# Kernel optimization log

Measured on AMD Instinct MI355X. Metric: run time of the kernel, lower is better.

## Reference

```python
import jax, jax.numpy as jnp
import numpy as np

NDIM = 3
IMG_SIZE = (192, 192, 192)
CPS = (5, 5, 5)
CP_GRID = (42, 42, 42)


def bspline_kernel_1d(stride):
    # cubic B-spline sampled at (i - radius)/stride, length 4*stride-1
    n = 4 * stride - 1
    t = np.abs((np.arange(n) - n // 2) / float(stride))
    vals = np.where(t < 1.0, 2.0 / 3.0 + (0.5 * t - 1.0) * t ** 2,
                    np.where(t < 2.0, -((t - 2.0) ** 3) / 6.0, 0.0))
    return jnp.asarray(vals, dtype=jnp.float32)


def conv_transpose1d_lastaxis(x, kernel, stride, padding):
    # depthwise transposed conv along last axis; same kernel for every channel,
    # so fold all leading dims into the batch and use a single-channel conv
    # with lhs_dilation (equivalent to conv_transpose; kernel is symmetric).
    shp = x.shape
    K = kernel.shape[0]
    x2 = x.reshape(-1, 1, shp[-1])  # [N, C=1, L]
    w = kernel.reshape(1, 1, K)     # [O, I, W]
    pad = K - 1 - padding
    y = jax.lax.conv_general_dilated(
        x2, w, window_strides=(1,), padding=[(pad, pad)],
        lhs_dilation=(stride,), dimension_numbers=("NCW", "OIW", "NCW"))
    return y.reshape(shp[:-1] + (y.shape[-1],))


def setup_inputs() -> dict:
    key = jax.random.key(0)
    v = jax.random.normal(key, (4, NDIM) + CP_GRID, dtype=jnp.float32)
    return {"v": v}


def reference(v) -> jnp.ndarray:
    kernels = [bspline_kernel_1d(s) for s in CPS]
    for i in range(NDIM):
        k = kernels[i]
        s = CPS[i]
        p = (k.shape[0] - 1) // 2
        x = jnp.moveaxis(v, i + 2, -1)
        x = conv_transpose1d_lastaxis(x, k, s, p)
        v = jnp.moveaxis(x, -1, i + 2)
    # crop: slice(s, s + img_size) per spatial dim
    slicer = (slice(None), slice(None)) + tuple(
        slice(CPS[i], CPS[i] + IMG_SIZE[i]) for i in range(NDIM))
    return v[slicer]
```

## Files before the change

kernel.cpp:

```cpp
#include <hip/hip_runtime.h>
#include <hip/hip_bf16.h>


#define CPN 42
#define IMG 192
#define TXX 6
#define TYY 6
#define NCX 5
#define NCY 5
#define NCZ 42
#define SXS 44
#define NTHREADS 256
#define ZBS 80
#define POOLF (TXX * TYY * ZBS)

struct WTabC { double w[5][4]; };
constexpr WTabC make_wb() {
  WTabC t{};
  for (int r = 0; r < 5; ++r) {
    double f = (double)r / 5.0;
    double g = (double)(5 - r) / 5.0;
    t.w[r][0] = g * g * g / 6.0;
    t.w[r][1] = 2.0 / 3.0 + (0.5 * f - 1.0) * f * f;
    t.w[r][2] = 2.0 / 3.0 + (0.5 * g - 1.0) * g * g;
    t.w[r][3] = f * f * f / 6.0;
  }
  return t;
}
constexpr WTabC WB = make_wb();

__device__ __forceinline__ float bsp_w_rt(int r, int d) {
  double f = (double)r / 5.0;
  double g = (double)(5 - r) / 5.0;
  double w;
  if (d == 0)      { w = g * g * g / 6.0; }
  else if (d == 1) { w = 2.0 / 3.0 + (0.5 * f - 1.0) * f * f; }
  else if (d == 2) { w = 2.0 / 3.0 + (0.5 * g - 1.0) * g * g; }
  else             { w = f * f * f / 6.0; }
  return (float)w;
}

template <int CB, int NC, int NQ>
__device__ __forceinline__ void z_chunk(const float* sxy_, float* zbuf,
                                        float* op, int x0, int y0, int tid) {
  for (int j = tid; j < TXX * TYY * NC; j += NTHREADS) {
    int cc = j % NC;
    int xy = j / NC;
    const float* sp = &sxy_[xy * SXS + CB + cc];
    float f0 = sp[0], f1 = sp[1], f2 = sp[2], f3 = sp[3];
    float* zp = &zbuf[xy * ZBS + 5 * cc];
#pragma unroll
    for (int r = 0; r < 5; ++r) {
      zp[r] = (float)WB.w[r][0] * f0 + (float)WB.w[r][1] * f1
            + (float)WB.w[r][2] * f2 + (float)WB.w[r][3] * f3;
    }
  }
  __syncthreads();
  for (int l = tid; l < TXX * TYY * NQ; l += NTHREADS) {
    int q = l % NQ;
    int xy = l / NQ;
    int yi = xy % TYY;
    int xi = xy / TYY;
    const float4 val =
        *reinterpret_cast<const float4*>(&zbuf[xy * ZBS + 4 * q]);
    float* dst = op + ((size_t)((x0 + xi) * IMG + (y0 + yi)) * IMG
                       + CB * 5 + 4 * q);
    *reinterpret_cast<float4*>(dst) = val;
  }
}

__global__ void __launch_bounds__(NTHREADS) ffd_kernel(
    const float* __restrict__ v, float* __restrict__ out) {
  const int tid = threadIdx.x;
  const int bx = blockIdx.x;
  const int by = blockIdx.y;
  const int sl = blockIdx.z;

  const int x0 = bx * TXX;
  const int y0 = by * TYY;
  const int cx0 = x0 / 5;
  const int cy0 = y0 / 5;

  __shared__ float wtab[20];
  __shared__ __align__(16) float sxy[TXX * TYY * SXS];
  __shared__ __align__(16) float pool[POOLF];
  float* vt = pool;
  float* t1 = pool + NCX * NCY * NCZ;

  if (tid < 20) wtab[tid] = bsp_w_rt(tid >> 2, tid & 3);

  const float* vs = v + (size_t)sl * (CPN * CPN * CPN);
  for (int l = tid; l < NCX * NCY * NCZ; l += NTHREADS) {
    int cz = l % NCZ;
    int rest = l / NCZ;
    int cy = rest % NCY;
    int cx = rest / NCY;
    vt[l] = vs[((cx0 + cx) * CPN + (cy0 + cy)) * CPN + cz];
  }
  __syncthreads();

  for (int l = tid; l < TYY * NCX * NCZ; l += NTHREADS) {
    int cz = l % NCZ;
    int rest = l / NCZ;
    int cx = rest % NCX;
    int yi = rest / NCX;
    int y = y0 + yi;
    int ay = y / 5;
    int ry = y - 5 * ay;
    int cyo = ay - cy0;
    const float* wr = &wtab[ry * 4];
    const float* vp = &vt[(cx * NCY + cyo) * NCZ + cz];
    float acc = wr[0] * vp[0] + wr[1] * vp[NCZ]
              + wr[2] * vp[2 * NCZ] + wr[3] * vp[3 * NCZ];
    t1[(yi * NCX + cx) * NCZ + cz] = acc;
  }
  __syncthreads();

  for (int l = tid; l < TXX * TYY * NCZ; l += NTHREADS) {
    int cz = l % NCZ;
    int rest = l / NCZ;
    int yi = rest % TYY;
    int xi = rest / TYY;
    int x = x0 + xi;
    int ax = x / 5;
    int rx = x - 5 * ax;
    int cxo = ax - cx0;
    const float* wr = &wtab[rx * 4];
    const float* tp = &t1[(yi * NCX + cxo) * NCZ + cz];
    float acc = wr[0] * tp[0] + wr[1] * tp[NCZ]
              + wr[2] * tp[2 * NCZ] + wr[3] * tp[3 * NCZ];
    sxy[(xi * TYY + yi) * SXS + cz] = acc;
  }
  __syncthreads();

  float* op = out + (size_t)sl * (IMG * IMG * IMG);
  z_chunk<0, 16, 20>(sxy, pool, op, x0, y0, tid);
  __syncthreads();
  z_chunk<16, 16, 20>(sxy, pool, op, x0, y0, tid);
  __syncthreads();
  z_chunk<32, 7, 8>(sxy, pool, op, x0, y0, tid);
}

extern "C" void kernel_launch(void* const* d_in, const int* in_sizes, int n_in,
                              void* d_out, int out_size, void* d_ws, size_t ws_size,
                              hipStream_t stream) {
  (void)in_sizes; (void)n_in; (void)d_ws; (void)ws_size; (void)out_size;
  const float* v = (const float*)d_in[0];
  float* out = (float*)d_out;
  dim3 grid(IMG / TXX, IMG / TYY, 12);
  ffd_kernel<<<grid, NTHREADS, 0, stream>>>(v, out);
}
```

Before: 364.1 us.

## Compute each output column per wavefront with cross-lane z-interpolation, dropping shared staging

Each wavefront now handles a whole (x,y) output column. Lanes load control points straight from global memory and do the x/y tensor interpolation in registers. The z interpolation exchanges neighbouring control values across lanes with ds_bpermute, and each lane writes a float4 of outputs. This removes the shared-memory staging of the control patch and intermediates, along with most block barriers. The cost is redundant global (cached) loads of 16 control points per column instead of reusing a shared tile, plus some idle lanes in each wave.

```diff
diff --git a/kernel.cpp b/kernel.cpp
--- a/kernel.cpp
+++ b/kernel.cpp
@@ -1,33 +1,12 @@
 #include <hip/hip_runtime.h>
-#include <hip/hip_bf16.h>
 
 
 #define CPN 42
 #define IMG 192
 #define TXX 6
 #define TYY 6
-#define NCX 5
-#define NCY 5
-#define NCZ 42
-#define SXS 44
 #define NTHREADS 256
-#define ZBS 80
-#define POOLF (TXX * TYY * ZBS)
-
-struct WTabC { double w[5][4]; };
-constexpr WTabC make_wb() {
-  WTabC t{};
-  for (int r = 0; r < 5; ++r) {
-    double f = (double)r / 5.0;
-    double g = (double)(5 - r) / 5.0;
-    t.w[r][0] = g * g * g / 6.0;
-    t.w[r][1] = 2.0 / 3.0 + (0.5 * f - 1.0) * f * f;
-    t.w[r][2] = 2.0 / 3.0 + (0.5 * g - 1.0) * g * g;
-    t.w[r][3] = f * f * f / 6.0;
-  }
-  return t;
-}
-constexpr WTabC WB = make_wb();
+#define SLICE (CPN * CPN * CPN)
 
 __device__ __forceinline__ float bsp_w_rt(int r, int d) {
   double f = (double)r / 5.0;
@@ -40,105 +19,91 @@
   return (float)w;
 }
 
-template <int CB, int NC, int NQ>
-__device__ __forceinline__ void z_chunk(const float* sxy_, float* zbuf,
-                                        float* op, int x0, int y0, int tid) {
-  for (int j = tid; j < TXX * TYY * NC; j += NTHREADS) {
-    int cc = j % NC;
-    int xy = j / NC;
-    const float* sp = &sxy_[xy * SXS + CB + cc];
-    float f0 = sp[0], f1 = sp[1], f2 = sp[2], f3 = sp[3];
-    float* zp = &zbuf[xy * ZBS + 5 * cc];
-#pragma unroll
-    for (int r = 0; r < 5; ++r) {
-      zp[r] = (float)WB.w[r][0] * f0 + (float)WB.w[r][1] * f1
-            + (float)WB.w[r][2] * f2 + (float)WB.w[r][3] * f3;
-    }
-  }
-  __syncthreads();
-  for (int l = tid; l < TXX * TYY * NQ; l += NTHREADS) {
-    int q = l % NQ;
-    int xy = l / NQ;
-    int yi = xy % TYY;
-    int xi = xy / TYY;
-    const float4 val =
-        *reinterpret_cast<const float4*>(&zbuf[xy * ZBS + 4 * q]);
-    float* dst = op + ((size_t)((x0 + xi) * IMG + (y0 + yi)) * IMG
-                       + CB * 5 + 4 * q);
-    *reinterpret_cast<float4*>(dst) = val;
-  }
-}
-
 __global__ void __launch_bounds__(NTHREADS) ffd_kernel(
     const float* __restrict__ v, float* __restrict__ out) {
   const int tid = threadIdx.x;
+  const int w = tid >> 6;
+  const int lane = tid & 63;
   const int bx = blockIdx.x;
   const int by = blockIdx.y;
   const int sl = blockIdx.z;
-
   const int x0 = bx * TXX;
   const int y0 = by * TYY;
-  const int cx0 = x0 / 5;
-  const int cy0 = y0 / 5;
 
   __shared__ float wtab[20];
-  __shared__ __align__(16) float sxy[TXX * TYY * SXS];
-  __shared__ __align__(16) float pool[POOLF];
-  float* vt = pool;
-  float* t1 = pool + NCX * NCY * NCZ;
-
   if (tid < 20) wtab[tid] = bsp_w_rt(tid >> 2, tid & 3);
-
-  const float* vs = v + (size_t)sl * (CPN * CPN * CPN);
-  for (int l = tid; l < NCX * NCY * NCZ; l += NTHREADS) {
-    int cz = l % NCZ;
-    int rest = l / NCZ;
-    int cy = rest % NCY;
-    int cx = rest / NCY;
-    vt[l] = vs[((cx0 + cx) * CPN + (cy0 + cy)) * CPN + cz];
-  }
   __syncthreads();
 
-  for (int l = tid; l < TYY * NCX * NCZ; l += NTHREADS) {
-    int cz = l % NCZ;
-    int rest = l / NCZ;
-    int cx = rest % NCX;
-    int yi = rest / NCX;
+  const int q = lane < 48 ? lane : 47;
+  const int c0 = (4 * q) / 5;
+  float wz[4][5];
+#pragma unroll
+  for (int k = 0; k < 4; ++k) {
+    int z = 4 * q + k;
+    int c = z / 5;
+    int r = z - 5 * c;
+    int off = c - c0;
+#pragma unroll
+    for (int t = 0; t < 5; ++t) {
+      int d = t - off;
+      wz[k][t] = (d >= 0 && d < 4) ? wtab[r * 4 + d] : 0.0f;
+    }
+  }
+
+  const float* vs = v + (size_t)sl * SLICE;
+  float* os = out + (size_t)sl * ((size_t)IMG * IMG * IMG);
+  const int cc = lane < 42 ? lane : 41;
+
+  for (int i = 0; i < 9; ++i) {
+    int col = w + 4 * i;
+    int xi = col / 6;
+    int yi = col - 6 * xi;
+    int x = x0 + xi;
     int y = y0 + yi;
-    int ay = y / 5;
-    int ry = y - 5 * ay;
-    int cyo = ay - cy0;
-    const float* wr = &wtab[ry * 4];
-    const float* vp = &vt[(cx * NCY + cyo) * NCZ + cz];
-    float acc = wr[0] * vp[0] + wr[1] * vp[NCZ]
-              + wr[2] * vp[2 * NCZ] + wr[3] * vp[3 * NCZ];
-    t1[(yi * NCX + cx) * NCZ + cz] = acc;
+    int ax = x / 5, rx = x - 5 * ax;
+    int ay = y / 5, ry = y - 5 * ay;
+    float wx0 = wtab[rx * 4 + 0], wx1 = wtab[rx * 4 + 1];
+    float wx2 = wtab[rx * 4 + 2], wx3 = wtab[rx * 4 + 3];
+    float wy0 = wtab[ry * 4 + 0], wy1 = wtab[ry * 4 + 1];
+    float wy2 = wtab[ry * 4 + 2], wy3 = wtab[ry * 4 + 3];
+
+    const float* vb = vs + (ax * CPN + ay) * CPN + cc;
+    float t2 = 0.0f;
+#pragma unroll
+    for (int dx = 0; dx < 4; ++dx) {
+      const float* vp = vb + dx * (CPN * CPN);
+      float s = wy0 * vp[0];
+      s = fmaf(wy1, vp[CPN], s);
+      s = fmaf(wy2, vp[2 * CPN], s);
+      s = fmaf(wy3, vp[3 * CPN], s);
+      float wx = (dx == 0) ? wx0 : (dx == 1) ? wx1 : (dx == 2) ? wx2 : wx3;
+      t2 = fmaf(wx, s, t2);
+    }
+
+    int t2i = __float_as_int(t2);
+    float s[5];
+#pragma unroll
+    for (int t = 0; t < 5; ++t)
+      s[t] = __int_as_float(
+          __builtin_amdgcn_ds_bpermute((c0 + t) << 2, t2i));
+
+    float res[4];
+#pragma unroll
+    for (int k = 0; k < 4; ++k) {
+      float a = wz[k][0] * s[0];
+      a = fmaf(wz[k][1], s[1], a);
+      a = fmaf(wz[k][2], s[2], a);
+      a = fmaf(wz[k][3], s[3], a);
+      a = fmaf(wz[k][4], s[4], a);
+      res[k] = a;
+    }
+
+    if (lane < 48) {
+      float4 val = make_float4(res[0], res[1], res[2], res[3]);
+      *reinterpret_cast<float4*>(
+          os + (size_t)(x * IMG + y) * IMG + 4 * lane) = val;
+    }
   }
-  __syncthreads();
-
-  for (int l = tid; l < TXX * TYY * NCZ; l += NTHREADS) {
-    int cz = l % NCZ;
-    int rest = l / NCZ;
-    int yi = rest % TYY;
-    int xi = rest / TYY;
-    int x = x0 + xi;
-    int ax = x / 5;
-    int rx = x - 5 * ax;
-    int cxo = ax - cx0;
-    const float* wr = &wtab[rx * 4];
-    const float* tp = &t1[(yi * NCX + cxo) * NCZ + cz];
-    float acc = wr[0] * tp[0] + wr[1] * tp[NCZ]
-              + wr[2] * tp[2 * NCZ] + wr[3] * tp[3 * NCZ];
-    sxy[(xi * TYY + yi) * SXS + cz] = acc;
-  }
-  __syncthreads();
-
-  float* op = out + (size_t)sl * (IMG * IMG * IMG);
-  z_chunk<0, 16, 20>(sxy, pool, op, x0, y0, tid);
-  __syncthreads();
-  z_chunk<16, 16, 20>(sxy, pool, op, x0, y0, tid);
-  __syncthreads();
-  z_chunk<32, 7, 8>(sxy, pool, op, x0, y0, tid);
 }
 
 extern "C" void kernel_launch(void* const* d_in, const int* in_sizes, int n_in,
```

Measured after the change: 386.0 us. 1.06x slower.

## Split FFD into xy stage and streaming z-expansion kernel using output as scratch

Applied to the files above, without the earlier changes.

The fused kernel is split in two. The first kernel keeps the x/y B-spline passes and writes the 44 z-control-point values per output column into the start of that column in the output buffer. A second grid-stride kernel assigns one wavefront per column. It reads the 5 needed coefficients per lane, computes 4 z outputs with precomputed per-lane weights, and writes them back in place with nontemporal float4 stores. This removes the shared-memory staging and the extra barriers of the z-chunk loop and gives a fully coalesced store stream. The cost is an extra launch and an extra write and read of the intermediate. It also depends on every lane loading before any lane stores within a column, since the update is in place.

```diff
diff --git a/kernel.cpp b/kernel.cpp
--- a/kernel.cpp
+++ b/kernel.cpp
@@ -1,5 +1,4 @@
 #include <hip/hip_runtime.h>
-#include <hip/hip_bf16.h>
 
 
 #define CPN 42
@@ -11,23 +10,11 @@
 #define NCZ 42
 #define SXS 44
 #define NTHREADS 256
-#define ZBS 80
-#define POOLF (TXX * TYY * ZBS)
+#define SLICE (CPN * CPN * CPN)
+#define NCOLS (12 * IMG * IMG)
+#define K2_BLOCKS 2048
 
-struct WTabC { double w[5][4]; };
-constexpr WTabC make_wb() {
-  WTabC t{};
-  for (int r = 0; r < 5; ++r) {
-    double f = (double)r / 5.0;
-    double g = (double)(5 - r) / 5.0;
-    t.w[r][0] = g * g * g / 6.0;
-    t.w[r][1] = 2.0 / 3.0 + (0.5 * f - 1.0) * f * f;
-    t.w[r][2] = 2.0 / 3.0 + (0.5 * g - 1.0) * g * g;
-    t.w[r][3] = f * f * f / 6.0;
-  }
-  return t;
-}
-constexpr WTabC WB = make_wb();
+typedef float v4f __attribute__((ext_vector_type(4)));
 
 __device__ __forceinline__ float bsp_w_rt(int r, int d) {
   double f = (double)r / 5.0;
@@ -40,56 +27,25 @@
   return (float)w;
 }
 
-template <int CB, int NC, int NQ>
-__device__ __forceinline__ void z_chunk(const float* sxy_, float* zbuf,
-                                        float* op, int x0, int y0, int tid) {
-  for (int j = tid; j < TXX * TYY * NC; j += NTHREADS) {
-    int cc = j % NC;
-    int xy = j / NC;
-    const float* sp = &sxy_[xy * SXS + CB + cc];
-    float f0 = sp[0], f1 = sp[1], f2 = sp[2], f3 = sp[3];
-    float* zp = &zbuf[xy * ZBS + 5 * cc];
-#pragma unroll
-    for (int r = 0; r < 5; ++r) {
-      zp[r] = (float)WB.w[r][0] * f0 + (float)WB.w[r][1] * f1
-            + (float)WB.w[r][2] * f2 + (float)WB.w[r][3] * f3;
-    }
-  }
-  __syncthreads();
-  for (int l = tid; l < TXX * TYY * NQ; l += NTHREADS) {
-    int q = l % NQ;
-    int xy = l / NQ;
-    int yi = xy % TYY;
-    int xi = xy / TYY;
-    const float4 val =
-        *reinterpret_cast<const float4*>(&zbuf[xy * ZBS + 4 * q]);
-    float* dst = op + ((size_t)((x0 + xi) * IMG + (y0 + yi)) * IMG
-                       + CB * 5 + 4 * q);
-    *reinterpret_cast<float4*>(dst) = val;
-  }
-}
-
-__global__ void __launch_bounds__(NTHREADS) ffd_kernel(
+__global__ void __launch_bounds__(NTHREADS) ffd_stage1(
     const float* __restrict__ v, float* __restrict__ out) {
   const int tid = threadIdx.x;
   const int bx = blockIdx.x;
   const int by = blockIdx.y;
   const int sl = blockIdx.z;
-
   const int x0 = bx * TXX;
   const int y0 = by * TYY;
   const int cx0 = x0 / 5;
   const int cy0 = y0 / 5;
 
   __shared__ float wtab[20];
+  __shared__ float vt[NCX * NCY * NCZ];
+  __shared__ float t1[TYY * NCX * NCZ];
   __shared__ __align__(16) float sxy[TXX * TYY * SXS];
-  __shared__ __align__(16) float pool[POOLF];
-  float* vt = pool;
-  float* t1 = pool + NCX * NCY * NCZ;
 
   if (tid < 20) wtab[tid] = bsp_w_rt(tid >> 2, tid & 3);
 
-  const float* vs = v + (size_t)sl * (CPN * CPN * CPN);
+  const float* vs = v + (size_t)sl * SLICE;
   for (int l = tid; l < NCX * NCY * NCZ; l += NTHREADS) {
     int cz = l % NCZ;
     int rest = l / NCZ;
@@ -133,12 +89,63 @@
   }
   __syncthreads();
 
-  float* op = out + (size_t)sl * (IMG * IMG * IMG);
-  z_chunk<0, 16, 20>(sxy, pool, op, x0, y0, tid);
-  __syncthreads();
-  z_chunk<16, 16, 20>(sxy, pool, op, x0, y0, tid);
-  __syncthreads();
-  z_chunk<32, 7, 8>(sxy, pool, op, x0, y0, tid);
+  float* os = out + (size_t)sl * ((size_t)IMG * IMG * IMG);
+  for (int l = tid; l < TXX * TYY * 11; l += NTHREADS) {
+    int qq = l % 11;
+    int xy = l / 11;
+    int yi = xy % TYY;
+    int xi = xy / TYY;
+    v4f val = *reinterpret_cast<const v4f*>(&sxy[xy * SXS + 4 * qq]);
+    *reinterpret_cast<v4f*>(
+        os + (size_t)((x0 + xi) * IMG + (y0 + yi)) * IMG + 4 * qq) = val;
+  }
+}
+
+__global__ void __launch_bounds__(NTHREADS) ffd_stage2(
+    const float* __restrict__ src, float* __restrict__ dst) {
+  const int lane = threadIdx.x & 63;
+  const int gw = (blockIdx.x * NTHREADS + threadIdx.x) >> 6;
+  const int nw = (K2_BLOCKS * NTHREADS) >> 6;
+
+  const int q = lane < 48 ? lane : 47;
+  const int c0 = (4 * q) / 5;
+  float wz[4][5];
+#pragma unroll
+  for (int k = 0; k < 4; ++k) {
+    int z = 4 * q + k;
+    int c = z / 5;
+    int r = z - 5 * c;
+    int off = c - c0;
+#pragma unroll
+    for (int t = 0; t < 5; ++t) {
+      int d = t - off;
+      wz[k][t] = (d >= 0 && d < 4) ? bsp_w_rt(r, d) : 0.0f;
+    }
+  }
+
+#pragma unroll 2
+  for (int n = gw; n < NCOLS; n += nw) {
+    const float* cp = src + (size_t)n * IMG;
+    float s0 = cp[c0];
+    float s1 = cp[c0 + 1];
+    float s2 = cp[c0 + 2];
+    float s3 = cp[c0 + 3];
+    float s4 = cp[c0 + 4];
+    v4f res;
+#pragma unroll
+    for (int k = 0; k < 4; ++k) {
+      float a = wz[k][0] * s0;
+      a = fmaf(wz[k][1], s1, a);
+      a = fmaf(wz[k][2], s2, a);
+      a = fmaf(wz[k][3], s3, a);
+      a = fmaf(wz[k][4], s4, a);
+      res[k] = a;
+    }
+    if (lane < 48) {
+      __builtin_nontemporal_store(
+          res, reinterpret_cast<v4f*>(dst + (size_t)n * IMG + 4 * q));
+    }
+  }
 }
 
 extern "C" void kernel_launch(void* const* d_in, const int* in_sizes, int n_in,
@@ -147,6 +154,7 @@
   (void)in_sizes; (void)n_in; (void)d_ws; (void)ws_size; (void)out_size;
   const float* v = (const float*)d_in[0];
   float* out = (float*)d_out;
-  dim3 grid(IMG / TXX, IMG / TYY, 12);
-  ffd_kernel<<<grid, NTHREADS, 0, stream>>>(v, out);
+  dim3 g1(IMG / TXX, IMG / TYY, 12);
+  ffd_stage1<<<g1, NTHREADS, 0, stream>>>(v, out);
+  ffd_stage2<<<K2_BLOCKS, NTHREADS, 0, stream>>>(out, out);
 }
```

After: 449.6 us. 23.5% more time.
